# Kernel tuning notes

Hardware: AMD Instinct MI355X
Metric: run time of the kernel (lower is better)

Reference implementation:

```python
import jax, jax.numpy as jnp
import numpy as np

B, N, D, K = 2, 4096, 1024, 256  # batch, seq, dim, low-rank k = dim//4


def setup_inputs() -> dict:
    key = jax.random.key(0)
    k1, k2, k3 = jax.random.split(key, 3)
    return {
        "x": jax.random.normal(k1, (B, N, D), dtype=jnp.float32),
        "compare_left": jax.random.normal(k2, (D, K), dtype=jnp.float32) * 0.05,
        "compare_right": jax.random.normal(k3, (D, K), dtype=jnp.float32) * 0.05,
        "threshold": jnp.zeros((1,), dtype=jnp.float32),
        "gate_bias": jnp.zeros((1,), dtype=jnp.float32),
    }


def reference(x, compare_left, compare_right, threshold, gate_bias):
    dim = x.shape[-1]
    left = x @ compare_left                     # [B, N, K]
    right = x @ compare_right                   # [B, N, K]
    # low-rank QK^T style comparison: [B, N, N]
    comparison = jnp.einsum('bik,bjk->bij', left, right) / jnp.sqrt(jnp.float32(dim))
    mask = (comparison > threshold).astype(x.dtype)
    gated = jax.nn.softmax(comparison + gate_bias, axis=-1)
    return (mask * gated) @ x                   # [B, N, D]
```

## Files before the change

kernel.cpp:

```cpp
#include <hip/hip_runtime.h>
#include <hip/hip_bf16.h>

#define B_  2
#define N_  4096
#define D_  1024
#define K_  256
#define NC_ 512

typedef __bf16 bf16;
typedef __bf16 bf16x8 __attribute__((ext_vector_type(8)));
typedef __bf16 bf16x4 __attribute__((ext_vector_type(4)));
typedef float  f32x4  __attribute__((ext_vector_type(4)));

#define MFMA(a, b, c) __builtin_amdgcn_mfma_f32_16x16x32_bf16(a, b, c, 0, 0, 0)

__device__ __forceinline__ void gload_lds16(const void* g, void* s) {
  __builtin_amdgcn_global_load_lds((const __attribute__((address_space(1))) void*)g,
                                   (__attribute__((address_space(3))) void*)s,
                                   16, 0, 0);
}

__global__ __launch_bounds__(256) void k_split_x(
    const float* __restrict__ x,
    bf16* __restrict__ xh,  bf16* __restrict__ xl,
    bf16* __restrict__ xth) {
  __shared__ bf16 th[32][33];
  int r0 = blockIdx.x * 32;
  int d0 = blockIdx.y * 32;
  int tc = threadIdx.x & 31, tr0 = threadIdx.x >> 5;
#pragma unroll
  for (int it = 0; it < 4; ++it) {
    int row = tr0 + it * 8;
    size_t idx = (size_t)(r0 + row) * D_ + d0 + tc;
    float f = x[idx];
    bf16 h = (bf16)f;
    bf16 l = (bf16)(f - (float)h);
    xh[idx] = h; xl[idx] = l;
    th[row][tc] = h;
  }
  __syncthreads();
  int b = r0 >> 12;
  int i0 = r0 & (N_ - 1);
#pragma unroll
  for (int it = 0; it < 4; ++it) {
    int dr = tr0 + it * 8;
    size_t idx = (size_t)b * D_ * N_ + (size_t)(d0 + dr) * N_ + i0 + tc;
    xth[idx] = th[tc][dr];
  }
}

__global__ __launch_bounds__(256) void k_split_c(
    const float* __restrict__ cl, const float* __restrict__ cr,
    bf16* __restrict__ cth, bf16* __restrict__ ctl) {
  __shared__ bf16 th[32][33], tl[32][33];
  int c0 = blockIdx.x * 32;
  int k0 = blockIdx.y * 32;
  int tc = threadIdx.x & 31, tr0 = threadIdx.x >> 5;
#pragma unroll
  for (int it = 0; it < 4; ++it) {
    int kk = tr0 + it * 8;
    int c = c0 + tc;
    float f = (c < K_) ? cl[(size_t)(k0 + kk) * K_ + c]
                       : cr[(size_t)(k0 + kk) * K_ + (c - K_)];
    bf16 h = (bf16)f;
    bf16 l = (bf16)(f - (float)h);
    th[kk][tc] = h; tl[kk][tc] = l;
  }
  __syncthreads();
#pragma unroll
  for (int it = 0; it < 4; ++it) {
    int cc = tr0 + it * 8;
    size_t idx = (size_t)(c0 + cc) * D_ + k0 + tc;
    cth[idx] = th[tc][cc];
    ctl[idx] = tl[tc][cc];
  }
}

__global__ __launch_bounds__(256) void k_proj(
    const bf16* __restrict__ xh, const bf16* __restrict__ xl,
    const bf16* __restrict__ cth, const bf16* __restrict__ ctl,
    bf16* __restrict__ lh, bf16* __restrict__ ll,
    bf16* __restrict__ rh, bf16* __restrict__ rl) {
  int tid = threadIdx.x, lane = tid & 63, wid = tid >> 6;
  int wm = wid >> 1, wn = wid & 1;
  int lr = lane & 15, lg = lane >> 4;
  int row0 = blockIdx.x * 128 + wm * 64;
  int col0 = blockIdx.y * 128 + wn * 64;
  f32x4 acc[4][4] = {};
  for (int ks = 0; ks < 32; ++ks) {
    int k = ks * 32 + lg * 8;
    bf16x8 Ah[4], Al[4], Bh[4], Bl[4];
#pragma unroll
    for (int mi = 0; mi < 4; ++mi) {
      size_t off = (size_t)(row0 + mi * 16 + lr) * D_ + k;
      Ah[mi] = *(const bf16x8*)(xh + off);
      Al[mi] = *(const bf16x8*)(xl + off);
    }
#pragma unroll
    for (int ni = 0; ni < 4; ++ni) {
      size_t off = (size_t)(col0 + ni * 16 + lr) * D_ + k;
      Bh[ni] = *(const bf16x8*)(cth + off);
      Bl[ni] = *(const bf16x8*)(ctl + off);
    }
#pragma unroll
    for (int mi = 0; mi < 4; ++mi)
#pragma unroll
      for (int ni = 0; ni < 4; ++ni) {
        acc[mi][ni] = MFMA(Ah[mi], Bh[ni], acc[mi][ni]);
        acc[mi][ni] = MFMA(Al[mi], Bh[ni], acc[mi][ni]);
        acc[mi][ni] = MFMA(Ah[mi], Bl[ni], acc[mi][ni]);
      }
  }
#pragma unroll
  for (int mi = 0; mi < 4; ++mi)
#pragma unroll
    for (int ni = 0; ni < 4; ++ni)
#pragma unroll
      for (int r = 0; r < 4; ++r) {
        int row = row0 + mi * 16 + lg * 4 + r;
        int col = col0 + ni * 16 + lr;
        float v = acc[mi][ni][r];
        bf16 h = (bf16)v;
        bf16 l = (bf16)(v - (float)h);
        if (col < K_) {
          lh[(size_t)row * K_ + col] = h;  ll[(size_t)row * K_ + col] = l;
        } else {
          rh[(size_t)row * K_ + col - K_] = h;  rl[(size_t)row * K_ + col - K_] = l;
        }
      }
}

__global__ __launch_bounds__(256) void k_qk(
    const bf16* __restrict__ lh, const bf16* __restrict__ ll,
    const bf16* __restrict__ rh, const bf16* __restrict__ rl,
    float* __restrict__ S) {
  int tid = threadIdx.x, lane = tid & 63, wid = tid >> 6;
  int wm = wid >> 1, wn = wid & 1;
  int lr = lane & 15, lg = lane >> 4;
  int b = blockIdx.z;
  int i0 = blockIdx.x * 128 + wm * 64;
  int j0 = blockIdx.y * 128 + wn * 64;
  const bf16* lhb = lh + (size_t)b * N_ * K_;
  const bf16* llb = ll + (size_t)b * N_ * K_;
  const bf16* rhb = rh + (size_t)b * N_ * K_;
  const bf16* rlb = rl + (size_t)b * N_ * K_;
  f32x4 acc[4][4] = {};
#pragma unroll
  for (int ks = 0; ks < 8; ++ks) {
    int k = ks * 32 + lg * 8;
    bf16x8 Ah[4], Al[4], Bh[4], Bl[4];
#pragma unroll
    for (int mi = 0; mi < 4; ++mi) {
      size_t off = (size_t)(i0 + mi * 16 + lr) * K_ + k;
      Ah[mi] = *(const bf16x8*)(lhb + off);
      Al[mi] = *(const bf16x8*)(llb + off);
    }
#pragma unroll
    for (int ni = 0; ni < 4; ++ni) {
      size_t off = (size_t)(j0 + ni * 16 + lr) * K_ + k;
      Bh[ni] = *(const bf16x8*)(rhb + off);
      Bl[ni] = *(const bf16x8*)(rlb + off);
    }
#pragma unroll
    for (int mi = 0; mi < 4; ++mi)
#pragma unroll
      for (int ni = 0; ni < 4; ++ni) {
        acc[mi][ni] = MFMA(Ah[mi], Bh[ni], acc[mi][ni]);
        acc[mi][ni] = MFMA(Al[mi], Bh[ni], acc[mi][ni]);
        acc[mi][ni] = MFMA(Ah[mi], Bl[ni], acc[mi][ni]);
      }
  }
  float* Sb = S + (size_t)b * N_ * N_;
  const float sc = 0.03125f;
#pragma unroll
  for (int mi = 0; mi < 4; ++mi)
#pragma unroll
    for (int ni = 0; ni < 4; ++ni)
#pragma unroll
      for (int r = 0; r < 4; ++r) {
        int row = i0 + mi * 16 + lg * 4 + r;
        int col = j0 + ni * 16 + lr;
        Sb[(size_t)row * N_ + col] = acc[mi][ni][r] * sc;
      }
}

__global__ __launch_bounds__(256) void k_stats_p(
    const float* __restrict__ S, const float* __restrict__ thrp,
    bf16* __restrict__ P) {
  int row = blockIdx.x;
  const float* sr = S + (size_t)row * N_;
  bf16* pr = P + (size_t)row * N_;
  int tid = threadIdx.x;
  float thr = *thrp;
  float4 v[4];
  float m = -3.4e38f;
#pragma unroll
  for (int it = 0; it < 4; ++it) {
    v[it] = *(const float4*)(sr + it * 1024 + tid * 4);
    m = fmaxf(m, fmaxf(fmaxf(v[it].x, v[it].y), fmaxf(v[it].z, v[it].w)));
  }
#pragma unroll
  for (int o = 32; o; o >>= 1) m = fmaxf(m, __shfl_xor(m, o, 64));
  __shared__ float wm_[4], ws_[4];
  __shared__ float sm, sil;
  int lane = tid & 63, wid = tid >> 6;
  if (lane == 0) wm_[wid] = m;
  __syncthreads();
  m = fmaxf(fmaxf(wm_[0], wm_[1]), fmaxf(wm_[2], wm_[3]));
  float l = 0.f;
#pragma unroll
  for (int it = 0; it < 4; ++it)
    l += __expf(v[it].x - m) + __expf(v[it].y - m) +
         __expf(v[it].z - m) + __expf(v[it].w - m);
#pragma unroll
  for (int o = 32; o; o >>= 1) l += __shfl_xor(l, o, 64);
  if (lane == 0) ws_[wid] = l;
  __syncthreads();
  if (tid == 0) {
    float lt = ws_[0] + ws_[1] + ws_[2] + ws_[3];
    sm = m; sil = 1.0f / lt;
  }
  __syncthreads();
  float mm = sm, il = sil;
#pragma unroll
  for (int it = 0; it < 4; ++it) {
    float p0 = (v[it].x > thr) ? __expf(v[it].x - mm) * il : 0.f;
    float p1 = (v[it].y > thr) ? __expf(v[it].y - mm) * il : 0.f;
    float p2 = (v[it].z > thr) ? __expf(v[it].z - mm) * il : 0.f;
    float p3 = (v[it].w > thr) ? __expf(v[it].w - mm) * il : 0.f;
    *(bf16x4*)(pr + it * 1024 + tid * 4) = (bf16x4){(bf16)p0, (bf16)p1, (bf16)p2, (bf16)p3};
  }
}

__global__ __launch_bounds__(256) void k_pv(
    const bf16* __restrict__ P, const bf16* __restrict__ VT,
    float* __restrict__ out) {
  __shared__ bf16 sA[2][128 * 32], sB[2][128 * 32];
  int tid = threadIdx.x, lane = tid & 63, wid = tid >> 6;
  int b = blockIdx.z;
  int i0 = blockIdx.x * 128, d0 = blockIdx.y * 128;
  const bf16* Ab = P + (size_t)b * N_ * N_;
  const bf16* Bb = VT + (size_t)b * D_ * N_;
  int wm = wid >> 1, wn = wid & 1;
  int lr = lane & 15, lg = lane >> 4;
  int srow = (lane >> 2);
  int scol = (lane & 3) * 8;

  f32x4 acc[4][4] = {};
  int cur = 0;

#pragma unroll
  for (int q = 0; q < 2; ++q) {
    int chunk = wid * 2 + q;
    gload_lds16(Ab + (size_t)(i0 + chunk * 16 + srow) * N_ + scol,
                &sA[0][chunk * 512]);
    gload_lds16(Bb + (size_t)(d0 + chunk * 16 + srow) * N_ + scol,
                &sB[0][chunk * 512]);
  }
  __syncthreads();

  for (int t = 0; t < N_ / 32; ++t) {
    if (t + 1 < N_ / 32) {
      int kk = (t + 1) * 32;
#pragma unroll
      for (int q = 0; q < 2; ++q) {
        int chunk = wid * 2 + q;
        gload_lds16(Ab + (size_t)(i0 + chunk * 16 + srow) * N_ + kk + scol,
                    &sA[cur ^ 1][chunk * 512]);
        gload_lds16(Bb + (size_t)(d0 + chunk * 16 + srow) * N_ + kk + scol,
                    &sB[cur ^ 1][chunk * 512]);
      }
    }
    bf16x8 Af[4], Bf[4];
#pragma unroll
    for (int mi = 0; mi < 4; ++mi)
      Af[mi] = *(const bf16x8*)&sA[cur][(wm * 64 + mi * 16 + lr) * 32 + lg * 8];
#pragma unroll
    for (int ni = 0; ni < 4; ++ni)
      Bf[ni] = *(const bf16x8*)&sB[cur][(wn * 64 + ni * 16 + lr) * 32 + lg * 8];
#pragma unroll
    for (int mi = 0; mi < 4; ++mi)
#pragma unroll
      for (int ni = 0; ni < 4; ++ni)
        acc[mi][ni] = MFMA(Af[mi], Bf[ni], acc[mi][ni]);
    __syncthreads();
    cur ^= 1;
  }

  float* ob = out + (size_t)b * N_ * D_;
#pragma unroll
  for (int mi = 0; mi < 4; ++mi)
#pragma unroll
    for (int ni = 0; ni < 4; ++ni)
#pragma unroll
      for (int r = 0; r < 4; ++r) {
        int row = i0 + wm * 64 + mi * 16 + lg * 4 + r;
        int col = d0 + wn * 64 + ni * 16 + lr;
        ob[(size_t)row * D_ + col] = acc[mi][ni][r];
      }
}

extern "C" void kernel_launch(void* const* d_in, const int* in_sizes, int n_in,
                              void* d_out, int out_size, void* d_ws, size_t ws_size,
                              hipStream_t stream) {
  const float* x   = (const float*)d_in[0];
  const float* cl  = (const float*)d_in[1];
  const float* cr  = (const float*)d_in[2];
  const float* thr = (const float*)d_in[3];
  float* out = (float*)d_out;

  char* w = (char*)d_ws;
  size_t off = 0;
  auto alloc = [&](size_t bytes) -> char* {
    char* p = w + off;
    off += (bytes + 255) & ~(size_t)255;
    return p;
  };
  const size_t XE = (size_t)B_ * N_ * D_;
  const size_t LRE = (size_t)B_ * N_ * K_;
  char* pool = alloc(64ull << 20);
  bf16* xh = (bf16*)pool;
  bf16* xl = (bf16*)(pool + (XE * 2));
  bf16* lh = (bf16*)(pool + (32ull << 20));
  bf16* ll = (bf16*)(pool + (32ull << 20) + LRE * 2);
  bf16* rh = (bf16*)(pool + (32ull << 20) + LRE * 4);
  bf16* rl = (bf16*)(pool + (32ull << 20) + LRE * 6);
  bf16* Ph = (bf16*)pool;
  bf16* xth = (bf16*)alloc(XE * 2);
  bf16* cth = (bf16*)alloc((size_t)NC_ * D_ * 2);
  bf16* ctl = (bf16*)alloc((size_t)NC_ * D_ * 2);
  float* S  = (float*)alloc((size_t)B_ * N_ * N_ * 4);

  k_split_x<<<dim3((B_ * N_) / 32, D_ / 32), 256, 0, stream>>>(x, xh, xl, xth);
  k_split_c<<<dim3(NC_ / 32, D_ / 32), 256, 0, stream>>>(cl, cr, cth, ctl);
  k_proj<<<dim3((B_ * N_) / 128, NC_ / 128), 256, 0, stream>>>(xh, xl, cth, ctl, lh, ll, rh, rl);
  k_qk<<<dim3(N_ / 128, N_ / 128, B_), 256, 0, stream>>>(lh, ll, rh, rl, S);
  k_stats_p<<<B_ * N_, 256, 0, stream>>>(S, thr, Ph);
  k_pv<<<dim3(N_ / 128, D_ / 128, B_), 256, 0, stream>>>(Ph, xth, out);
}
```

Measured before the change: 432.6 us.

## Interleave hi/lo splits and stage proj/qk GEMMs through double-buffered LDS

The hi and lo bf16 splits of x, the weights and the projections are packed into shared rows, so the three-term split product becomes one longer K loop over concatenated segments. The projection and QK GEMMs now load tiles into LDS with async global-to-LDS copies and double buffering, instead of each wave reading operands straight from global memory. This aims to cut redundant global loads and raise MFMA utilisation, at the cost of a barrier every tile and three times as many K-steps through shared memory.

```diff
diff --git a/kernel.cpp b/kernel.cpp
--- a/kernel.cpp
+++ b/kernel.cpp
@@ -22,8 +22,7 @@
 
 __global__ __launch_bounds__(256) void k_split_x(
     const float* __restrict__ x,
-    bf16* __restrict__ xh,  bf16* __restrict__ xl,
-    bf16* __restrict__ xth) {
+    bf16* __restrict__ X2, bf16* __restrict__ xth) {
   __shared__ bf16 th[32][33];
   int r0 = blockIdx.x * 32;
   int d0 = blockIdx.y * 32;
@@ -35,7 +34,8 @@
     float f = x[idx];
     bf16 h = (bf16)f;
     bf16 l = (bf16)(f - (float)h);
-    xh[idx] = h; xl[idx] = l;
+    size_t base = (size_t)(r0 + row) * 2048 + d0 + tc;
+    X2[base] = h; X2[base + 1024] = l;
     th[row][tc] = h;
   }
   __syncthreads();
@@ -51,7 +51,7 @@
 
 __global__ __launch_bounds__(256) void k_split_c(
     const float* __restrict__ cl, const float* __restrict__ cr,
-    bf16* __restrict__ cth, bf16* __restrict__ ctl) {
+    bf16* __restrict__ C2) {
   __shared__ bf16 th[32][33], tl[32][33];
   int c0 = blockIdx.x * 32;
   int k0 = blockIdx.y * 32;
@@ -70,46 +70,59 @@
 #pragma unroll
   for (int it = 0; it < 4; ++it) {
     int cc = tr0 + it * 8;
-    size_t idx = (size_t)(c0 + cc) * D_ + k0 + tc;
-    cth[idx] = th[tc][cc];
-    ctl[idx] = tl[tc][cc];
+    size_t base = (size_t)(c0 + cc) * 2048 + k0 + tc;
+    C2[base] = th[tc][cc];
+    C2[base + 1024] = tl[tc][cc];
   }
 }
 
 __global__ __launch_bounds__(256) void k_proj(
-    const bf16* __restrict__ xh, const bf16* __restrict__ xl,
-    const bf16* __restrict__ cth, const bf16* __restrict__ ctl,
-    bf16* __restrict__ lh, bf16* __restrict__ ll,
-    bf16* __restrict__ rh, bf16* __restrict__ rl) {
+    const bf16* __restrict__ X2, const bf16* __restrict__ C2,
+    bf16* __restrict__ L2, bf16* __restrict__ R2) {
+  __shared__ bf16 sA[2][128 * 32], sB[2][128 * 32];
   int tid = threadIdx.x, lane = tid & 63, wid = tid >> 6;
+  int row0 = blockIdx.x * 128, col0 = blockIdx.y * 128;
   int wm = wid >> 1, wn = wid & 1;
   int lr = lane & 15, lg = lane >> 4;
-  int row0 = blockIdx.x * 128 + wm * 64;
-  int col0 = blockIdx.y * 128 + wn * 64;
+  int srow = lane >> 2, scol = (lane & 3) * 8;
   f32x4 acc[4][4] = {};
-  for (int ks = 0; ks < 32; ++ks) {
-    int k = ks * 32 + lg * 8;
-    bf16x8 Ah[4], Al[4], Bh[4], Bl[4];
-#pragma unroll
-    for (int mi = 0; mi < 4; ++mi) {
-      size_t off = (size_t)(row0 + mi * 16 + lr) * D_ + k;
-      Ah[mi] = *(const bf16x8*)(xh + off);
-      Al[mi] = *(const bf16x8*)(xl + off);
+  int cur = 0;
+  const int NT = 96;
+#pragma unroll
+  for (int q = 0; q < 2; ++q) {
+    int chunk = wid * 2 + q;
+    gload_lds16(X2 + (size_t)(row0 + chunk * 16 + srow) * 2048 + scol, &sA[0][chunk * 512]);
+    gload_lds16(C2 + (size_t)(col0 + chunk * 16 + srow) * 2048 + scol, &sB[0][chunk * 512]);
+  }
+  __syncthreads();
+  for (int t = 0; t < NT; ++t) {
+    if (t + 1 < NT) {
+      int tn = t + 1, tm = tn & 31, grp = tn >> 5;
+      int aO = tm * 32 + (grp == 1 ? 1024 : 0);
+      int bO = tm * 32 + (grp == 2 ? 1024 : 0);
+#pragma unroll
+      for (int q = 0; q < 2; ++q) {
+        int chunk = wid * 2 + q;
+        gload_lds16(X2 + (size_t)(row0 + chunk * 16 + srow) * 2048 + aO + scol,
+                    &sA[cur ^ 1][chunk * 512]);
+        gload_lds16(C2 + (size_t)(col0 + chunk * 16 + srow) * 2048 + bO + scol,
+                    &sB[cur ^ 1][chunk * 512]);
+      }
     }
-#pragma unroll
-    for (int ni = 0; ni < 4; ++ni) {
-      size_t off = (size_t)(col0 + ni * 16 + lr) * D_ + k;
-      Bh[ni] = *(const bf16x8*)(cth + off);
-      Bl[ni] = *(const bf16x8*)(ctl + off);
-    }
-#pragma unroll
-    for (int mi = 0; mi < 4; ++mi)
-#pragma unroll
-      for (int ni = 0; ni < 4; ++ni) {
-        acc[mi][ni] = MFMA(Ah[mi], Bh[ni], acc[mi][ni]);
-        acc[mi][ni] = MFMA(Al[mi], Bh[ni], acc[mi][ni]);
-        acc[mi][ni] = MFMA(Ah[mi], Bl[ni], acc[mi][ni]);
-      }
+    bf16x8 Af[4], Bf[4];
+#pragma unroll
+    for (int mi = 0; mi < 4; ++mi)
+      Af[mi] = *(const bf16x8*)&sA[cur][(wm * 64 + mi * 16 + lr) * 32 + lg * 8];
+#pragma unroll
+    for (int ni = 0; ni < 4; ++ni)
+      Bf[ni] = *(const bf16x8*)&sB[cur][(wn * 64 + ni * 16 + lr) * 32 + lg * 8];
+#pragma unroll
+    for (int mi = 0; mi < 4; ++mi)
+#pragma unroll
+      for (int ni = 0; ni < 4; ++ni)
+        acc[mi][ni] = MFMA(Af[mi], Bf[ni], acc[mi][ni]);
+    __syncthreads();
+    cur ^= 1;
   }
 #pragma unroll
   for (int mi = 0; mi < 4; ++mi)
@@ -117,58 +130,71 @@
     for (int ni = 0; ni < 4; ++ni)
 #pragma unroll
       for (int r = 0; r < 4; ++r) {
-        int row = row0 + mi * 16 + lg * 4 + r;
-        int col = col0 + ni * 16 + lr;
+        int row = row0 + wm * 64 + mi * 16 + lg * 4 + r;
+        int col = col0 + wn * 64 + ni * 16 + lr;
         float v = acc[mi][ni][r];
         bf16 h = (bf16)v;
         bf16 l = (bf16)(v - (float)h);
         if (col < K_) {
-          lh[(size_t)row * K_ + col] = h;  ll[(size_t)row * K_ + col] = l;
+          L2[(size_t)row * 512 + col] = h;
+          L2[(size_t)row * 512 + col + 256] = l;
         } else {
-          rh[(size_t)row * K_ + col - K_] = h;  rl[(size_t)row * K_ + col - K_] = l;
+          R2[(size_t)row * 512 + col - 256] = h;
+          R2[(size_t)row * 512 + col] = l;
         }
       }
 }
 
 __global__ __launch_bounds__(256) void k_qk(
-    const bf16* __restrict__ lh, const bf16* __restrict__ ll,
-    const bf16* __restrict__ rh, const bf16* __restrict__ rl,
+    const bf16* __restrict__ L2, const bf16* __restrict__ R2,
     float* __restrict__ S) {
+  __shared__ bf16 sA[2][128 * 32], sB[2][128 * 32];
   int tid = threadIdx.x, lane = tid & 63, wid = tid >> 6;
+  int b = blockIdx.z;
+  int i0 = blockIdx.x * 128, j0 = blockIdx.y * 128;
+  const bf16* Ab = L2 + (size_t)b * N_ * 512;
+  const bf16* Bb = R2 + (size_t)b * N_ * 512;
   int wm = wid >> 1, wn = wid & 1;
   int lr = lane & 15, lg = lane >> 4;
-  int b = blockIdx.z;
-  int i0 = blockIdx.x * 128 + wm * 64;
-  int j0 = blockIdx.y * 128 + wn * 64;
-  const bf16* lhb = lh + (size_t)b * N_ * K_;
-  const bf16* llb = ll + (size_t)b * N_ * K_;
-  const bf16* rhb = rh + (size_t)b * N_ * K_;
-  const bf16* rlb = rl + (size_t)b * N_ * K_;
+  int srow = lane >> 2, scol = (lane & 3) * 8;
   f32x4 acc[4][4] = {};
-#pragma unroll
-  for (int ks = 0; ks < 8; ++ks) {
-    int k = ks * 32 + lg * 8;
-    bf16x8 Ah[4], Al[4], Bh[4], Bl[4];
-#pragma unroll
-    for (int mi = 0; mi < 4; ++mi) {
-      size_t off = (size_t)(i0 + mi * 16 + lr) * K_ + k;
-      Ah[mi] = *(const bf16x8*)(lhb + off);
-      Al[mi] = *(const bf16x8*)(llb + off);
+  int cur = 0;
+  const int NT = 24;
+#pragma unroll
+  for (int q = 0; q < 2; ++q) {
+    int chunk = wid * 2 + q;
+    gload_lds16(Ab + (size_t)(i0 + chunk * 16 + srow) * 512 + scol, &sA[0][chunk * 512]);
+    gload_lds16(Bb + (size_t)(j0 + chunk * 16 + srow) * 512 + scol, &sB[0][chunk * 512]);
+  }
+  __syncthreads();
+  for (int t = 0; t < NT; ++t) {
+    if (t + 1 < NT) {
+      int tn = t + 1, tm = tn & 7, grp = tn >> 3;
+      int aO = tm * 32 + (grp == 1 ? 256 : 0);
+      int bO = tm * 32 + (grp == 2 ? 256 : 0);
+#pragma unroll
+      for (int q = 0; q < 2; ++q) {
+        int chunk = wid * 2 + q;
+        gload_lds16(Ab + (size_t)(i0 + chunk * 16 + srow) * 512 + aO + scol,
+                    &sA[cur ^ 1][chunk * 512]);
+        gload_lds16(Bb + (size_t)(j0 + chunk * 16 + srow) * 512 + bO + scol,
+                    &sB[cur ^ 1][chunk * 512]);
+      }
     }
-#pragma unroll
-    for (int ni = 0; ni < 4; ++ni) {
-      size_t off = (size_t)(j0 + ni * 16 + lr) * K_ + k;
-      Bh[ni] = *(const bf16x8*)(rhb + off);
-      Bl[ni] = *(const bf16x8*)(rlb + off);
-    }
-#pragma unroll
-    for (int mi = 0; mi < 4; ++mi)
-#pragma unroll
-      for (int ni = 0; ni < 4; ++ni) {
-        acc[mi][ni] = MFMA(Ah[mi], Bh[ni], acc[mi][ni]);
-        acc[mi][ni] = MFMA(Al[mi], Bh[ni], acc[mi][ni]);
-        acc[mi][ni] = MFMA(Ah[mi], Bl[ni], acc[mi][ni]);
-      }
+    bf16x8 Af[4], Bf[4];
+#pragma unroll
+    for (int mi = 0; mi < 4; ++mi)
+      Af[mi] = *(const bf16x8*)&sA[cur][(wm * 64 + mi * 16 + lr) * 32 + lg * 8];
+#pragma unroll
+    for (int ni = 0; ni < 4; ++ni)
+      Bf[ni] = *(const bf16x8*)&sB[cur][(wn * 64 + ni * 16 + lr) * 32 + lg * 8];
+#pragma unroll
+    for (int mi = 0; mi < 4; ++mi)
+#pragma unroll
+      for (int ni = 0; ni < 4; ++ni)
+        acc[mi][ni] = MFMA(Af[mi], Bf[ni], acc[mi][ni]);
+    __syncthreads();
+    cur ^= 1;
   }
   float* Sb = S + (size_t)b * N_ * N_;
   const float sc = 0.03125f;
@@ -178,8 +204,8 @@
     for (int ni = 0; ni < 4; ++ni)
 #pragma unroll
       for (int r = 0; r < 4; ++r) {
-        int row = i0 + mi * 16 + lg * 4 + r;
-        int col = j0 + ni * 16 + lr;
+        int row = i0 + wm * 64 + mi * 16 + lg * 4 + r;
+        int col = j0 + wn * 64 + ni * 16 + lr;
         Sb[(size_t)row * N_ + col] = acc[mi][ni][r] * sc;
       }
 }
@@ -252,10 +278,8 @@
 #pragma unroll
   for (int q = 0; q < 2; ++q) {
     int chunk = wid * 2 + q;
-    gload_lds16(Ab + (size_t)(i0 + chunk * 16 + srow) * N_ + scol,
-                &sA[0][chunk * 512]);
-    gload_lds16(Bb + (size_t)(d0 + chunk * 16 + srow) * N_ + scol,
-                &sB[0][chunk * 512]);
+    gload_lds16(Ab + (size_t)(i0 + chunk * 16 + srow) * N_ + scol, &sA[0][chunk * 512]);
+    gload_lds16(Bb + (size_t)(d0 + chunk * 16 + srow) * N_ + scol, &sB[0][chunk * 512]);
   }
   __syncthreads();
 
@@ -317,24 +341,19 @@
     return p;
   };
   const size_t XE = (size_t)B_ * N_ * D_;
-  const size_t LRE = (size_t)B_ * N_ * K_;
   char* pool = alloc(64ull << 20);
-  bf16* xh = (bf16*)pool;
-  bf16* xl = (bf16*)(pool + (XE * 2));
-  bf16* lh = (bf16*)(pool + (32ull << 20));
-  bf16* ll = (bf16*)(pool + (32ull << 20) + LRE * 2);
-  bf16* rh = (bf16*)(pool + (32ull << 20) + LRE * 4);
-  bf16* rl = (bf16*)(pool + (32ull << 20) + LRE * 6);
+  bf16* X2 = (bf16*)pool;
+  bf16* L2 = (bf16*)(pool + (32ull << 20));
+  bf16* R2 = (bf16*)(pool + (40ull << 20));
   bf16* Ph = (bf16*)pool;
   bf16* xth = (bf16*)alloc(XE * 2);
-  bf16* cth = (bf16*)alloc((size_t)NC_ * D_ * 2);
-  bf16* ctl = (bf16*)alloc((size_t)NC_ * D_ * 2);
+  bf16* C2  = (bf16*)alloc((size_t)NC_ * 2048 * 2);
   float* S  = (float*)alloc((size_t)B_ * N_ * N_ * 4);
 
-  k_split_x<<<dim3((B_ * N_) / 32, D_ / 32), 256, 0, stream>>>(x, xh, xl, xth);
-  k_split_c<<<dim3(NC_ / 32, D_ / 32), 256, 0, stream>>>(cl, cr, cth, ctl);
-  k_proj<<<dim3((B_ * N_) / 128, NC_ / 128), 256, 0, stream>>>(xh, xl, cth, ctl, lh, ll, rh, rl);
-  k_qk<<<dim3(N_ / 128, N_ / 128, B_), 256, 0, stream>>>(lh, ll, rh, rl, S);
+  k_split_x<<<dim3((B_ * N_) / 32, D_ / 32), 256, 0, stream>>>(x, X2, xth);
+  k_split_c<<<dim3(NC_ / 32, D_ / 32), 256, 0, stream>>>(cl, cr, C2);
+  k_proj<<<dim3((B_ * N_) / 128, NC_ / 128), 256, 0, stream>>>(X2, C2, L2, R2);
+  k_qk<<<dim3(N_ / 128, N_ / 128, B_), 256, 0, stream>>>(L2, R2, S);
   k_stats_p<<<B_ * N_, 256, 0, stream>>>(S, thr, Ph);
   k_pv<<<dim3(N_ / 128, D_ / 128, B_), 256, 0, stream>>>(Ph, xth, out);
 }
```

Result: faster. 375.2 us (-13.3%).
